# Kernel tuning notes

Hardware: AMD Instinct MI355X
Metric: run time of the kernel (lower is better)

## Reference

```python
import jax, jax.numpy as jnp
import numpy as np

STRIDE = 2

def setup_inputs() -> dict:
    key = jax.random.key(0)
    k1, k2 = jax.random.split(key)
    x = jax.random.normal(k1, (32, 128, 112, 112), dtype=jnp.float32)
    # matches nn.init.normal_(std=0.1)
    weight = jax.random.normal(k2, (256, 128, 3, 3), dtype=jnp.float32) * 0.1
    return {"x": x, "weight": weight}

def reference(x, weight):
    # Equivalent to the tile-loop: valid cross-correlation, no bias, stride=STRIDE.
    # x: (B, Cin, H, W); weight: (Cout, Cin, k, k) -> (B, Cout, w, w)
    return jax.lax.conv_general_dilated(
        x, weight,
        window_strides=(STRIDE, STRIDE),
        padding="VALID",
        dimension_numbers=("NCHW", "OIHW", "NCHW"),
    )
```

## Files before the change

### kernel.cpp

```cpp
#include <hip/hip_runtime.h>


#define BATCH 32
#define CIN   128
#define H     112
#define W     112
#define COUT  256
#define OH    55
#define OW    55
#define NPIX  (OH*OW)
#define NTOT  (BATCH*NPIX)

typedef __bf16 bf16x8 __attribute__((ext_vector_type(8)));
typedef float  f32x4  __attribute__((ext_vector_type(4)));

__device__ __forceinline__ unsigned short f2bf(float f) {
    unsigned u = __float_as_uint(f);
    u += 0x7FFFu + ((u >> 16) & 1u);
    return (unsigned short)(u >> 16);
}

__device__ __forceinline__ void gld_lds16(const void* g, void* l) {
    __builtin_amdgcn_global_load_lds((__attribute__((address_space(1))) void*)g,
                                     (__attribute__((address_space(3))) void*)l,
                                     16, 0, 0);
}

__global__ __launch_bounds__(256) void relayout_w_k(const float* __restrict__ w,
                                                    unsigned short* __restrict__ wt) {
    int o = blockIdx.x * 256 + threadIdx.x;
    if (o >= 9 * COUT * CIN) return;
    int cin  = o & (CIN - 1);
    int r    = o >> 7;
    int cout = r & (COUT - 1);
    int tap  = r >> 8;
    wt[o] = f2bf(w[((size_t)cout * CIN + cin) * 9 + tap]);
}

#define XP 136
__global__ __launch_bounds__(256) void relayout_x_k(const float* __restrict__ x,
                                                    unsigned short* __restrict__ xs) {
    __shared__ __align__(16) unsigned short tile[W * XP];
    const int bh = blockIdx.x;
    const int b  = bh / H;
    const int h  = bh - b * H;
    const float* xr = x + (size_t)b * CIN * (H * W) + (size_t)h * W;
    const int t = threadIdx.x;
#pragma unroll
    for (int i = 0; i < 14; ++i) {
        int e  = t + i * 256;
        int c  = e / 28;
        int w4 = e - c * 28;
        float4 v = *(const float4*)(xr + (size_t)c * (H * W) + w4 * 4);
        int base = (w4 * 4) * XP + c;
        tile[base]          = f2bf(v.x);
        tile[base + XP]     = f2bf(v.y);
        tile[base + 2 * XP] = f2bf(v.z);
        tile[base + 3 * XP] = f2bf(v.w);
    }
    __syncthreads();
    uint4* dst = (uint4*)(xs + (size_t)bh * (W * CIN));
#pragma unroll
    for (int i = 0; i < 7; ++i) {
        int e  = t + i * 256;
        int w  = e >> 4;
        int c8 = e & 15;
        dst[e] = *(const uint4*)(tile + w * XP + c8 * 8);
    }
}

__global__ __launch_bounds__(256) void conv_mfma_k(const unsigned short* __restrict__ xs,
                                                   const unsigned short* __restrict__ wt,
                                                   float* __restrict__ out) {
    __shared__ __align__(16) unsigned short Alds[2][128 * 32];
    __shared__ __align__(16) unsigned short Blds[2][128 * 32];

    const int t    = threadIdx.x;
    const int wave = t >> 6;
    const int lane = t & 63;
    const int m0   = blockIdx.y * 128;
    const int n0   = blockIdx.x * 128;

    const int srow = t >> 2;
    const int scol = (t & 3) * 8;

    int xb[2];
#pragma unroll
    for (int i = 0; i < 2; ++i) {
        int nn = n0 + srow + i * 64;
        if (nn >= NTOT) nn = NTOT - 1;
        int b  = nn / NPIX;
        int rp = nn - b * NPIX;
        int oh = rp / OW;
        int ow = rp - oh * OW;
        xb[i] = ((b * H + 2 * oh) * W + 2 * ow) * CIN;
    }

    const int lrow   = lane & 15;
    const int koff   = (lane >> 4) * 8;
    const int wave_m = (wave & 1) * 64;
    const int wave_n = (wave >> 1) * 64;

    f32x4 acc[4][4];
#pragma unroll
    for (int mi = 0; mi < 4; ++mi)
#pragma unroll
        for (int ni = 0; ni < 4; ++ni)
            acc[mi][ni] = (f32x4){0.f, 0.f, 0.f, 0.f};

    auto issue = [&](int ks, int buf) {
        int tap  = ks >> 2;
        int cin0 = (ks & 3) * 32;
        int r    = (tap >= 6) ? 2 : (tap >= 3) ? 1 : 0;
        int s    = tap - 3 * r;
        int toff = (r * W + s) * CIN;
        const unsigned short* wtap = wt + tap * (COUT * CIN) + (m0 + srow) * CIN + scol + cin0;
        const unsigned short* xst  = xs + toff + scol + cin0;
        unsigned short* la = &Alds[buf][0] + wave * 512;
        unsigned short* lb = &Blds[buf][0] + wave * 512;
        gld_lds16(wtap,             la);
        gld_lds16(wtap + 64 * CIN,  la + 2048);
        gld_lds16(xst + xb[0],      lb);
        gld_lds16(xst + xb[1],      lb + 2048);
    };

    issue(0, 0);
#pragma unroll 2
    for (int ks = 0; ks < 36; ++ks) {
        const int buf = ks & 1;
        __syncthreads();
        if (ks + 1 < 36) issue(ks + 1, buf ^ 1);

        bf16x8 af[4], bfr[4];
#pragma unroll
        for (int mi = 0; mi < 4; ++mi)
            af[mi] = *(const bf16x8*)(&Alds[buf][0] + (wave_m + mi * 16 + lrow) * 32 + koff);
#pragma unroll
        for (int ni = 0; ni < 4; ++ni)
            bfr[ni] = *(const bf16x8*)(&Blds[buf][0] + (wave_n + ni * 16 + lrow) * 32 + koff);
#pragma unroll
        for (int mi = 0; mi < 4; ++mi)
#pragma unroll
            for (int ni = 0; ni < 4; ++ni)
                acc[mi][ni] = __builtin_amdgcn_mfma_f32_16x16x32_bf16(af[mi], bfr[ni], acc[mi][ni], 0, 0, 0);
    }

    long obase[4];
    int  okn[4];
#pragma unroll
    for (int ni = 0; ni < 4; ++ni) {
        int nn = n0 + wave_n + ni * 16 + lrow;
        okn[ni] = (nn < NTOT);
        if (!okn[ni]) nn = 0;
        int b   = nn / NPIX;
        int pix = nn - b * NPIX;
        obase[ni] = (long)b * (COUT * NPIX) + pix;
    }
    const int mrow = (lane >> 4) * 4;
#pragma unroll
    for (int mi = 0; mi < 4; ++mi) {
#pragma unroll
        for (int rr = 0; rr < 4; ++rr) {
            int  m  = m0 + wave_m + mi * 16 + mrow + rr;
            long mo = (long)m * NPIX;
#pragma unroll
            for (int ni = 0; ni < 4; ++ni)
                if (okn[ni]) out[obase[ni] + mo] = acc[mi][ni][rr];
        }
    }
}

__global__ __launch_bounds__(256) void direct_k(const float* __restrict__ x,
                                                const float* __restrict__ w,
                                                float* __restrict__ out) {
    const int pix = blockIdx.x * 256 + threadIdx.x;
    if (pix >= NPIX) return;
    const int b = blockIdx.z, cout0 = blockIdx.y * 8;
    const int oh = pix / OW, ow = pix - oh * OW;
    float acc[8];
#pragma unroll
    for (int i = 0; i < 8; ++i) acc[i] = 0.f;
    const float* xbp = x + ((size_t)b * CIN) * (H * W) + (size_t)(oh * 2) * W + ow * 2;
    const float* wb  = w + (size_t)cout0 * (CIN * 9);
    for (int cin = 0; cin < CIN; ++cin) {
        const float* xp = xbp + (size_t)cin * (H * W);
        float xv[9];
#pragma unroll
        for (int r = 0; r < 3; ++r) {
            xv[r * 3 + 0] = xp[r * W + 0];
            xv[r * 3 + 1] = xp[r * W + 1];
            xv[r * 3 + 2] = xp[r * W + 2];
        }
#pragma unroll
        for (int c = 0; c < 8; ++c) {
            const float* wp = wb + (size_t)c * (CIN * 9) + cin * 9;
#pragma unroll
            for (int k = 0; k < 9; ++k) acc[c] = fmaf(wp[k], xv[k], acc[c]);
        }
    }
    const size_t ob = ((size_t)b * COUT + cout0) * NPIX + pix;
#pragma unroll
    for (int c = 0; c < 8; ++c) out[ob + (size_t)c * NPIX] = acc[c];
}

extern "C" void kernel_launch(void* const* d_in, const int* in_sizes, int n_in,
                              void* d_out, int out_size, void* d_ws, size_t ws_size,
                              hipStream_t stream) {
    const float* x = (const float*)d_in[0];
    const float* w = (const float*)d_in[1];
    float* out = (float*)d_out;

    const size_t xs_elems = (size_t)BATCH * H * W * CIN;
    const size_t wt_elems = (size_t)9 * COUT * CIN;
    const size_t need = (xs_elems + wt_elems) * 2;

    if (ws_size >= need) {
        unsigned short* xs = (unsigned short*)d_ws;
        unsigned short* wt = xs + xs_elems;
        relayout_w_k<<<(9 * COUT * CIN + 255) / 256, 256, 0, stream>>>(w, wt);
        relayout_x_k<<<BATCH * H, 256, 0, stream>>>(x, xs);
        dim3 grid((NTOT + 127) / 128, COUT / 128);
        conv_mfma_k<<<grid, dim3(256), 0, stream>>>(xs, wt, out);
    } else {
        dim3 grid((NPIX + 255) / 256, COUT / 8, BATCH);
        direct_k<<<grid, dim3(256), 0, stream>>>(x, w, out);
    }
}
```

Measured before the change: 410.3 us.

## Enlarge conv GEMM tile to full Cout x 192, swizzle LDS, merge relayout kernels

Each conv block now covers all 256 output channels against 192 pixels, using 512 threads and a K step of 64. Loads go through XOR-swizzled LDS with a two-deep prefetch, explicit vmcnt waits and barriers, and raised priority around the MFMA sections. The two relayout kernels are merged into one launch, and the x transpose now writes channel pairs into a swizzled tile to cut LDS bank conflicts. The aim is more reuse per load, fewer launches and better overlap of loads with MFMA, at the cost of higher register and LDS pressure, which may limit occupancy.

```diff
diff --git a/kernel.cpp b/kernel.cpp
--- a/kernel.cpp
+++ b/kernel.cpp
@@ -11,6 +11,9 @@
 #define NPIX  (OH*OW)
 #define NTOT  (BATCH*NPIX)
 
+#define BN    192
+#define NBLK  ((NTOT + BN - 1) / BN)
+
 typedef __bf16 bf16x8 __attribute__((ext_vector_type(8)));
 typedef float  f32x4  __attribute__((ext_vector_type(4)));
 
@@ -26,20 +29,23 @@
                                      16, 0, 0);
 }
 
-__global__ __launch_bounds__(256) void relayout_w_k(const float* __restrict__ w,
-                                                    unsigned short* __restrict__ wt) {
-    int o = blockIdx.x * 256 + threadIdx.x;
-    if (o >= 9 * COUT * CIN) return;
-    int cin  = o & (CIN - 1);
-    int r    = o >> 7;
-    int cout = r & (COUT - 1);
-    int tap  = r >> 8;
-    wt[o] = f2bf(w[((size_t)cout * CIN + cin) * 9 + tap]);
-}
-
 #define XP 136
-__global__ __launch_bounds__(256) void relayout_x_k(const float* __restrict__ x,
-                                                    unsigned short* __restrict__ xs) {
+#define WBLK ((9*COUT*CIN + 255)/256)
+__global__ __launch_bounds__(256) void relayout_k(const float* __restrict__ x,
+                                                  const float* __restrict__ w,
+                                                  unsigned short* __restrict__ xs,
+                                                  unsigned short* __restrict__ wt) {
+    if (blockIdx.x >= BATCH * H) {
+        int o = (blockIdx.x - BATCH * H) * 256 + threadIdx.x;
+        if (o < 9 * COUT * CIN) {
+            int cin  = o & (CIN - 1);
+            int r    = o >> 7;
+            int cout = r & (COUT - 1);
+            int tap  = r >> 8;
+            wt[o] = f2bf(w[((size_t)cout * CIN + cin) * 9 + tap]);
+        }
+        return;
+    }
     __shared__ __align__(16) unsigned short tile[W * XP];
     const int bh = blockIdx.x;
     const int b  = bh / H;
@@ -47,124 +53,154 @@
     const float* xr = x + (size_t)b * CIN * (H * W) + (size_t)h * W;
     const int t = threadIdx.x;
 #pragma unroll
-    for (int i = 0; i < 14; ++i) {
+    for (int i = 0; i < 7; ++i) {
         int e  = t + i * 256;
-        int c  = e / 28;
-        int w4 = e - c * 28;
-        float4 v = *(const float4*)(xr + (size_t)c * (H * W) + w4 * 4);
-        int base = (w4 * 4) * XP + c;
-        tile[base]          = f2bf(v.x);
-        tile[base + XP]     = f2bf(v.y);
-        tile[base + 2 * XP] = f2bf(v.z);
-        tile[base + 3 * XP] = f2bf(v.w);
+        int cp = e / 28;
+        int w4 = e - cp * 28;
+        int c  = cp * 2;
+        float4 v0 = *(const float4*)(xr + (size_t)c * (H * W) + w4 * 4);
+        float4 v1 = *(const float4*)(xr + (size_t)(c + 1) * (H * W) + w4 * 4);
+        int c8 = c >> 3;
+        int cl = c & 7;
+        float a0[4] = {v0.x, v0.y, v0.z, v0.w};
+        float a1[4] = {v1.x, v1.y, v1.z, v1.w};
+#pragma unroll
+        for (int j = 0; j < 4; ++j) {
+            int ww  = w4 * 4 + j;
+            int idx = ww * XP + ((c8 + 2 * ww) & 15) * 8 + cl;
+            *(ushort2*)(tile + idx) = (ushort2){f2bf(a0[j]), f2bf(a1[j])};
+        }
     }
     __syncthreads();
     uint4* dst = (uint4*)(xs + (size_t)bh * (W * CIN));
 #pragma unroll
     for (int i = 0; i < 7; ++i) {
         int e  = t + i * 256;
-        int w  = e >> 4;
+        int ww = e >> 4;
         int c8 = e & 15;
-        dst[e] = *(const uint4*)(tile + w * XP + c8 * 8);
-    }
-}
-
-__global__ __launch_bounds__(256) void conv_mfma_k(const unsigned short* __restrict__ xs,
-                                                   const unsigned short* __restrict__ wt,
-                                                   float* __restrict__ out) {
-    __shared__ __align__(16) unsigned short Alds[2][128 * 32];
-    __shared__ __align__(16) unsigned short Blds[2][128 * 32];
-
-    const int t    = threadIdx.x;
-    const int wave = t >> 6;
-    const int lane = t & 63;
-    const int m0   = blockIdx.y * 128;
-    const int n0   = blockIdx.x * 128;
-
-    const int srow = t >> 2;
-    const int scol = (t & 3) * 8;
-
-    int xb[2];
-#pragma unroll
-    for (int i = 0; i < 2; ++i) {
-        int nn = n0 + srow + i * 64;
+        dst[e] = *(const uint4*)(tile + ww * XP + ((c8 + 2 * ww) & 15) * 8);
+    }
+}
+
+__global__ __launch_bounds__(512, 2) void conv_mfma_k(const unsigned short* __restrict__ xs,
+                                                      const unsigned short* __restrict__ wt,
+                                                      float* __restrict__ out) {
+    __shared__ __align__(16) unsigned short L[2][(COUT + BN) * 64];
+
+    const int tid  = threadIdx.x;
+    const int wave = tid >> 6;
+    const int lane = tid & 63;
+    const int wm   = wave >> 2;
+    const int wn   = wave & 3;
+    const int lrow = lane & 15;
+    const int kg   = lane >> 4;
+    const int n0   = blockIdx.x * BN;
+
+    const int rA  = tid >> 3;
+    const int sx8 = ((tid & 7) ^ (rA & 7)) * 8;
+    int xbr[3];
+#pragma unroll
+    for (int c = 0; c < 3; ++c) {
+        int nn = n0 + c * 64 + rA;
         if (nn >= NTOT) nn = NTOT - 1;
         int b  = nn / NPIX;
         int rp = nn - b * NPIX;
         int oh = rp / OW;
         int ow = rp - oh * OW;
-        xb[i] = ((b * H + 2 * oh) * W + 2 * ow) * CIN;
-    }
-
-    const int lrow   = lane & 15;
-    const int koff   = (lane >> 4) * 8;
-    const int wave_m = (wave & 1) * 64;
-    const int wave_n = (wave >> 1) * 64;
-
-    f32x4 acc[4][4];
-#pragma unroll
-    for (int mi = 0; mi < 4; ++mi)
-#pragma unroll
-        for (int ni = 0; ni < 4; ++ni)
+        xbr[c] = ((b * H + 2 * oh) * W + 2 * ow) * CIN;
+    }
+
+    auto stage = [&](int kt, int buf) {
+        const int tap  = kt >> 1;
+        const int cin0 = (kt & 1) * 64;
+        const int r    = (tap >= 6) ? 2 : (tap >= 3) ? 1 : 0;
+        const int s    = tap - 3 * r;
+        const unsigned short* wsrc = wt + tap * (COUT * CIN) + rA * CIN + cin0 + sx8;
+        const unsigned short* xsrc = xs + (r * W + s) * CIN + cin0 + sx8;
+        unsigned short* lb = &L[buf][0];
+#pragma unroll
+        for (int c = 0; c < 4; ++c)
+            gld_lds16(wsrc + c * 64 * CIN, lb + c * 4096 + wave * 512);
+#pragma unroll
+        for (int c = 0; c < 3; ++c)
+            gld_lds16(xsrc + xbr[c], lb + 16384 + c * 4096 + wave * 512);
+    };
+
+    const int aoff = (wm * 128 + lrow) * 64;
+    const int boff = COUT * 64 + (wn * 48 + lrow) * 64;
+    const int sxk0 = ((0 * 4 + kg) ^ (lrow & 7)) * 8;
+    const int sxk1 = ((1 * 4 + kg) ^ (lrow & 7)) * 8;
+
+    f32x4 acc[8][3];
+#pragma unroll
+    for (int mi = 0; mi < 8; ++mi)
+#pragma unroll
+        for (int ni = 0; ni < 3; ++ni)
             acc[mi][ni] = (f32x4){0.f, 0.f, 0.f, 0.f};
 
-    auto issue = [&](int ks, int buf) {
-        int tap  = ks >> 2;
-        int cin0 = (ks & 3) * 32;
-        int r    = (tap >= 6) ? 2 : (tap >= 3) ? 1 : 0;
-        int s    = tap - 3 * r;
-        int toff = (r * W + s) * CIN;
-        const unsigned short* wtap = wt + tap * (COUT * CIN) + (m0 + srow) * CIN + scol + cin0;
-        const unsigned short* xst  = xs + toff + scol + cin0;
-        unsigned short* la = &Alds[buf][0] + wave * 512;
-        unsigned short* lb = &Blds[buf][0] + wave * 512;
-        gld_lds16(wtap,             la);
-        gld_lds16(wtap + 64 * CIN,  la + 2048);
-        gld_lds16(xst + xb[0],      lb);
-        gld_lds16(xst + xb[1],      lb + 2048);
-    };
-
-    issue(0, 0);
+    stage(0, 0);
+    stage(1, 1);
+
 #pragma unroll 2
-    for (int ks = 0; ks < 36; ++ks) {
-        const int buf = ks & 1;
-        __syncthreads();
-        if (ks + 1 < 36) issue(ks + 1, buf ^ 1);
-
-        bf16x8 af[4], bfr[4];
-#pragma unroll
-        for (int mi = 0; mi < 4; ++mi)
-            af[mi] = *(const bf16x8*)(&Alds[buf][0] + (wave_m + mi * 16 + lrow) * 32 + koff);
-#pragma unroll
-        for (int ni = 0; ni < 4; ++ni)
-            bfr[ni] = *(const bf16x8*)(&Blds[buf][0] + (wave_n + ni * 16 + lrow) * 32 + koff);
-#pragma unroll
-        for (int mi = 0; mi < 4; ++mi)
-#pragma unroll
-            for (int ni = 0; ni < 4; ++ni)
-                acc[mi][ni] = __builtin_amdgcn_mfma_f32_16x16x32_bf16(af[mi], bfr[ni], acc[mi][ni], 0, 0, 0);
-    }
-
-    long obase[4];
-    int  okn[4];
-#pragma unroll
-    for (int ni = 0; ni < 4; ++ni) {
-        int nn = n0 + wave_n + ni * 16 + lrow;
+    for (int kt = 0; kt < 18; ++kt) {
+        const int buf = kt & 1;
+        if (kt == 17) asm volatile("s_waitcnt vmcnt(0)" ::: "memory");
+        else          asm volatile("s_waitcnt vmcnt(7)" ::: "memory");
+        asm volatile("s_barrier" ::: "memory");
+
+        const unsigned short* Lb = &L[buf][0];
+        bf16x8 a0[8], b0[3], a1[8], b1[3];
+#pragma unroll
+        for (int mi = 0; mi < 8; ++mi)
+            a0[mi] = *(const bf16x8*)(Lb + aoff + mi * 1024 + sxk0);
+#pragma unroll
+        for (int ni = 0; ni < 3; ++ni)
+            b0[ni] = *(const bf16x8*)(Lb + boff + ni * 1024 + sxk0);
+        asm volatile("s_barrier" ::: "memory");
+#pragma unroll
+        for (int mi = 0; mi < 8; ++mi)
+            a1[mi] = *(const bf16x8*)(Lb + aoff + mi * 1024 + sxk1);
+#pragma unroll
+        for (int ni = 0; ni < 3; ++ni)
+            b1[ni] = *(const bf16x8*)(Lb + boff + ni * 1024 + sxk1);
+        __builtin_amdgcn_s_setprio(1);
+#pragma unroll
+        for (int mi = 0; mi < 8; ++mi)
+#pragma unroll
+            for (int ni = 0; ni < 3; ++ni)
+                acc[mi][ni] = __builtin_amdgcn_mfma_f32_16x16x32_bf16(a0[mi], b0[ni], acc[mi][ni], 0, 0, 0);
+        __builtin_amdgcn_s_setprio(0);
+        asm volatile("s_barrier" ::: "memory");
+        if (kt + 2 < 18) stage(kt + 2, buf);
+        __builtin_amdgcn_s_setprio(1);
+#pragma unroll
+        for (int mi = 0; mi < 8; ++mi)
+#pragma unroll
+            for (int ni = 0; ni < 3; ++ni)
+                acc[mi][ni] = __builtin_amdgcn_mfma_f32_16x16x32_bf16(a1[mi], b1[ni], acc[mi][ni], 0, 0, 0);
+        __builtin_amdgcn_s_setprio(0);
+    }
+
+    long obase[3];
+    int  okn[3];
+#pragma unroll
+    for (int ni = 0; ni < 3; ++ni) {
+        int nn = n0 + wn * 48 + ni * 16 + lrow;
         okn[ni] = (nn < NTOT);
         if (!okn[ni]) nn = 0;
         int b   = nn / NPIX;
         int pix = nn - b * NPIX;
         obase[ni] = (long)b * (COUT * NPIX) + pix;
     }
-    const int mrow = (lane >> 4) * 4;
-#pragma unroll
-    for (int mi = 0; mi < 4; ++mi) {
+    const int mrow = kg * 4;
+#pragma unroll
+    for (int mi = 0; mi < 8; ++mi) {
 #pragma unroll
         for (int rr = 0; rr < 4; ++rr) {
-            int  m  = m0 + wave_m + mi * 16 + mrow + rr;
+            int  m  = wm * 128 + mi * 16 + mrow + rr;
             long mo = (long)m * NPIX;
 #pragma unroll
-            for (int ni = 0; ni < 4; ++ni)
+            for (int ni = 0; ni < 3; ++ni)
                 if (okn[ni]) out[obase[ni] + mo] = acc[mi][ni][rr];
         }
     }
@@ -217,10 +253,8 @@
     if (ws_size >= need) {
         unsigned short* xs = (unsigned short*)d_ws;
         unsigned short* wt = xs + xs_elems;
-        relayout_w_k<<<(9 * COUT * CIN + 255) / 256, 256, 0, stream>>>(w, wt);
-        relayout_x_k<<<BATCH * H, 256, 0, stream>>>(x, xs);
-        dim3 grid((NTOT + 127) / 128, COUT / 128);
-        conv_mfma_k<<<grid, dim3(256), 0, stream>>>(xs, wt, out);
+        relayout_k<<<dim3(BATCH * H + WBLK), dim3(256), 0, stream>>>(x, w, xs, wt);
+        conv_mfma_k<<<dim3(NBLK), dim3(512), 0, stream>>>(xs, wt, out);
     } else {
         dim3 grid((NPIX + 255) / 256, COUT / 8, BATCH);
         direct_k<<<grid, dim3(256), 0, stream>>>(x, w, out);
```

New measurement: 382.3 us. 1.07x faster.
